# Kernel tuning notes

Hardware: AMD Instinct MI355X
Metric: run time of the kernel (lower is better)

Reference implementation:

```python
import jax, jax.numpy as jnp
import numpy as np

B, L, D = 32, 2048, 512
MODES = 32
H = 1           # num_head
E = D // H      # per-head channels
KMA = 128       # moving_avg kernel
EPS = 1e-5


def setup_inputs() -> dict:
    key = jax.random.key(0)
    ks = jax.random.split(key, 12)
    scale = 1.0 / (D * D)
    lin = lambda k, fi, fo: jax.random.uniform(k, (fo, fi), jnp.float32, -1, 1) / np.sqrt(fi)
    return {
        "x": jax.random.normal(ks[0], (B, L, D), jnp.float32),
        "W_in": lin(ks[1], D, H * E),
        "b_in": jnp.zeros((H * E,), jnp.float32),
        "Wf_r": scale * jax.random.uniform(ks[2], (H, E, E, MODES), jnp.float32),
        "Wf_i": scale * jax.random.uniform(ks[3], (H, E, E, MODES), jnp.float32),
        "W_out": lin(ks[4], H * E, D),
        "b_out": jnp.zeros((D,), jnp.float32),
        "W_conv1": lin(ks[5], D, D),
        "W_conv2": lin(ks[6], D, D),
        "bn_gamma": jnp.ones((L,), jnp.float32),
        "bn_beta": jnp.zeros((L,), jnp.float32),
    }


def moving_average(x, k):
    # x: (b, l, c); replicate-pad front/end exactly as the torch module, then avg-pool k/stride 1
    front = jnp.repeat(x[:, :1, :], k - 1 - (k - 1) // 2, axis=1)
    end = jnp.repeat(x[:, -1:, :], (k - 1) // 2, axis=1)
    xp = jnp.concatenate([front, x, end], axis=1)          # (b, l+k-1, c)
    cs = jnp.cumsum(xp, axis=1)
    cs = jnp.concatenate([jnp.zeros_like(cs[:, :1]), cs], axis=1)
    return (cs[:, k:] - cs[:, :-k]) / k                    # (b, l, c)


def reference(x, W_in, b_in, Wf_r, Wf_i, W_out, b_out, W_conv1, W_conv2, bn_gamma, bn_beta):
    b, l, d = x.shape
    # in projection -> (b, l, h, e) -> (b, h, e, l)
    q = x @ W_in.T + b_in
    q = q.reshape(b, l, H, E).transpose(0, 2, 3, 1)
    # FourierBlock: rfft over time, keep lowest MODES modes, complex mix, irfft
    x_ft = jnp.fft.rfft(q, axis=-1)                        # (b, h, e, l//2+1)
    Wf = (Wf_r + 1j * Wf_i).astype(x_ft.dtype)             # (h, e, e, m)
    out_modes = jnp.einsum('bhim,hiom->bhom', x_ft[..., :MODES], Wf)
    out_ft = jnp.pad(out_modes, ((0, 0), (0, 0), (0, 0), (0, l // 2 + 1 - MODES)))
    fre = jnp.fft.irfft(out_ft, n=l, axis=-1)              # (b, h, e, l)
    # (b, h, e, l) -> (b, l, h*e), out projection (dropout is eval-mode identity)
    fre = fre.transpose(0, 3, 1, 2).reshape(b, l, H * E)
    fre = fre @ W_out.T + b_out
    xr = x + fre
    # series decomposition 1: keep residual
    xr = xr - moving_average(xr, KMA)
    # conv1x1 -> gelu -> conv1x1 (exact erf gelu, matching F.gelu default)
    y = jax.nn.gelu(jnp.einsum('bld,ed->ble', xr, W_conv1), approximate=False)
    y = jnp.einsum('bld,ed->ble', y, W_conv2)
    res = xr + y
    # BatchNorm1d(in_len): channel axis is the time axis, batch stats over (b, d)
    mean = res.mean(axis=(0, 2), keepdims=True)
    var = ((res - mean) ** 2).mean(axis=(0, 2), keepdims=True)
    out = bn_gamma[None, :, None] * (res - mean) / jnp.sqrt(var + EPS) + bn_beta[None, :, None]
    return out
```

## Files before the change

kernel.cpp:

```cpp
#include <hip/hip_runtime.h>
#include <hip/hip_bf16.h>
#include <math.h>

#define B_   32
#define L_   2048
#define D_   512
#define BLROWS (B_*L_)
#define NBIG ((size_t)BLROWS * D_)

typedef __hip_bfloat16 bf16;
using bf16x8 = __attribute__((ext_vector_type(8))) short;
using f32x4  = __attribute__((ext_vector_type(4))) float;

__device__ __forceinline__ unsigned short f2b(float f) {
  bf16 h = __float2bfloat16(f);
  return *reinterpret_cast<unsigned short*>(&h);
}
__device__ __forceinline__ float b2f(unsigned short u) {
  union { unsigned int i; float f; } c;
  c.i = ((unsigned int)u) << 16;
  return c.f;
}

__device__ __forceinline__ void gl_lds16(const void* g, void* l) {
  __builtin_amdgcn_global_load_lds(
      (const __attribute__((address_space(1))) void*)g,
      (__attribute__((address_space(3))) void*)l, 16, 0, 0);
}

__global__ __launch_bounds__(256) void f2bfK(const float4* __restrict__ src,
                                             ushort4* __restrict__ dst,
                                             size_t n4) {
  for (size_t i = (size_t)blockIdx.x * 256 + threadIdx.x; i < n4;
       i += (size_t)gridDim.x * 256) {
    float4 v = src[i];
    ushort4 o;
    o.x = f2b(v.x); o.y = f2b(v.y); o.z = f2b(v.z); o.w = f2b(v.w);
    dst[i] = o;
  }
}

__global__ __launch_bounds__(256) void genTwCS(bf16* __restrict__ TwCS) {
  int idx = blockIdx.x * 256 + threadIdx.x;
  int mrow = idx >> 11, l = idx & 2047;
  int m = mrow & 31;
  int r = (m * l) & (L_ - 1);
  float ang = (float)r * (6.283185307179586f / (float)L_);
  TwCS[idx] = __float2bfloat16((mrow < 32) ? cosf(ang) : -sinf(ang));
}

__global__ __launch_bounds__(256) void genTbF(float* __restrict__ Tb) {
  int idx = blockIdx.x * 256 + threadIdx.x;
  int l = idx >> 6, j = idx & 63;
  int m = j >> 1;
  int r = (m * l) & (L_ - 1);
  float ang = (float)r * (6.283185307179586f / (float)L_);
  Tb[idx] = (j & 1) ? sinf(ang) : cosf(ang);
}

__global__ __launch_bounds__(256) void genTbDbf(const float* __restrict__ Tb,
                                                bf16* __restrict__ TbD) {
  int idx = blockIdx.x * 256 + threadIdx.x;
  int l = idx >> 6, j = idx & 63;
  float s = 0.f;
  for (int t = l - 64; t < l + 64; t++) {
    int cl = min(max(t, 0), L_ - 1);
    s += Tb[cl * 64 + j];
  }
  TbD[idx] = __float2bfloat16(Tb[idx] - s * (1.f / 128.f));
}

__global__ __launch_bounds__(256) void twWf2(const float* __restrict__ Wfr,
                                             const float* __restrict__ Wfi,
                                             bf16* __restrict__ Wcat2) {
  __shared__ __align__(16) bf16 st[256 * 72];
  const int t = threadIdx.x;
  const int i0 = blockIdx.x * 64, o0 = blockIdx.y * 8;
  const int arr = blockIdx.z;
  const float* src = arr ? Wfi : Wfr;
#pragma unroll
  for (int s8 = 0; s8 < 8; s8++) {
    unsigned short v[8];
#pragma unroll
    for (int ss = 0; ss < 8; ss++)
      v[ss] = f2b(src[(size_t)(i0 + s8 * 8 + ss) * 16384 + o0 * 32 + t]);
    int4 wv;
    wv.x = (int)v[0] | ((int)v[1] << 16);
    wv.y = (int)v[2] | ((int)v[3] << 16);
    wv.z = (int)v[4] | ((int)v[5] << 16);
    wv.w = (int)v[6] | ((int)v[7] << 16);
    *(int4*)&st[t * 72 + s8 * 8] = wv;
  }
  __syncthreads();
#pragma unroll
  for (int p = 0; p < 8; p++) {
    const int om = p * 32 + (t >> 3), c = t & 7;
    const int o = om >> 5, m = om & 31;
    int4 rv = *(const int4*)&st[om * 72 + c * 8];
    bf16* dst = Wcat2 + (size_t)m * 524288 + (size_t)(o0 + o) * 1024 +
                arr * 512 + i0 + c * 8;
    *(int4*)dst = rv;
  }
}

template <bool GELU, bool RESID, bool BIAS, bool OUTBF, bool RESBF, bool AFP32,
          bool DFTE>
__global__ __launch_bounds__(256) void gemm_k64(
    const void* __restrict__ Av, const bf16* __restrict__ Wt,
    const float* __restrict__ bias, const void* __restrict__ resid,
    void* __restrict__ Cout, int M, int N, int K,
    const bf16* __restrict__ TwCS, bf16* __restrict__ Pdft) {
  __shared__ __align__(16) bf16 As[2][128 * 64];
  __shared__ __align__(16) bf16 Bs[2][128 * 64];
  const int t = threadIdx.x;
  const int lane = t & 63;
  const int w = t >> 6, wr = w >> 1, wc = w & 1;

  const int id = blockIdx.x;
  const int xcd = id & 7, rest = id >> 3;
  const int cb = rest & 3, rg = rest >> 2;
  const int row0 = (rg * 8 + xcd) * 128, col0 = cb * 128;

  const bf16* Ab = (const bf16*)Av;
  const float* Af = (const float*)Av;

  f32x4 acc[4][4];
#pragma unroll
  for (int i = 0; i < 4; i++)
#pragma unroll
    for (int j = 0; j < 4; j++) acc[i][j] = (f32x4){0.f, 0.f, 0.f, 0.f};

  auto stage = [&](int buf, int k0) {
#pragma unroll
    for (int s = 0; s < 4; s++) {
      const int ci = s * 256 + t;
      const int row = ci >> 3;
      const int cg = ci & 7;
      const int pc = cg ^ (row & 7);
      if (AFP32) {
        const float* ax = Af + (size_t)(row0 + row) * K + k0 + cg * 8;
        float4 v0 = *(const float4*)(ax);
        float4 v1 = *(const float4*)(ax + 4);
        int4 wv;
        wv.x = (int)f2b(v0.x) | ((int)f2b(v0.y) << 16);
        wv.y = (int)f2b(v0.z) | ((int)f2b(v0.w) << 16);
        wv.z = (int)f2b(v1.x) | ((int)f2b(v1.y) << 16);
        wv.w = (int)f2b(v1.z) | ((int)f2b(v1.w) << 16);
        *(int4*)&As[buf][(size_t)(row * 8 + pc) * 8] = wv;
      } else {
        const int kqg = cg ^ (row & 7);
        bf16* dA = &As[buf][(size_t)(s * 256 + (t & ~63)) * 8];
        gl_lds16(Ab + (size_t)(row0 + row) * K + k0 + kqg * 8, dA);
      }
      {
        const int kqg = cg ^ (row & 7);
        bf16* dB = &Bs[buf][(size_t)(s * 256 + (t & ~63)) * 8];
        gl_lds16(Wt + (size_t)(col0 + row) * K + k0 + kqg * 8, dB);
      }
    }
  };

  stage(0, 0);
  int cur = 0;
  for (int k0 = 0; k0 < K; k0 += 64) {
    __syncthreads();
    if (k0 + 64 < K) stage(cur ^ 1, k0 + 64);
#pragma unroll
    for (int ks = 0; ks < 2; ks++) {
      const int c = ks * 4 + (lane >> 4);
      const int pc = c ^ (lane & 7);
      bf16x8 af[4], bg[4];
#pragma unroll
      for (int m = 0; m < 4; m++) {
        const int ra = wr * 64 + m * 16 + (lane & 15);
        af[m] = *reinterpret_cast<const bf16x8*>(&As[cur][(ra * 8 + pc) * 8]);
      }
#pragma unroll
      for (int n = 0; n < 4; n++) {
        const int rb = wc * 64 + n * 16 + (lane & 15);
        bg[n] = *reinterpret_cast<const bf16x8*>(&Bs[cur][(rb * 8 + pc) * 8]);
      }
#pragma unroll
      for (int n = 0; n < 4; n++)
#pragma unroll
        for (int m = 0; m < 4; m++)
          acc[n][m] = __builtin_amdgcn_mfma_f32_16x16x32_bf16(
              bg[n], af[m], acc[n][m], 0, 0, 0);
    }
    cur ^= 1;
  }

  if (DFTE) {
    bf16* QT = (bf16*)As;
    __syncthreads();
#pragma unroll
    for (int n = 0; n < 4; n++) {
      const int ibase = wc * 64 + n * 16 + ((lane >> 4) << 2);
      float4 bsv = *(const float4*)(bias + col0 + ibase);
#pragma unroll
      for (int m = 0; m < 4; m++) {
        const int lloc = wr * 64 + m * 16 + (lane & 15);
#pragma unroll
        for (int j = 0; j < 4; j++) {
          const int iloc = ibase + j;
          float u = acc[n][m][j] + (&bsv.x)[j];
          QT[iloc * 128 + (((lloc >> 3) ^ (iloc & 7)) << 3) + (lloc & 7)] =
              __float2bfloat16(u);
        }
      }
    }
    __syncthreads();
    const int bidx = row0 >> 11, lblk = (row0 >> 7) & 15;
    const int l0g = row0 & 2047;
    f32x4 accd[4][2];
#pragma unroll
    for (int mp = 0; mp < 4; mp++)
#pragma unroll
      for (int ip = 0; ip < 2; ip++) accd[mp][ip] = (f32x4){0.f,0.f,0.f,0.f};
#pragma unroll
    for (int kc = 0; kc < 4; kc++) {
      bf16x8 bgt[4], afq[2];
#pragma unroll
      for (int mp = 0; mp < 4; mp++)
        bgt[mp] = *reinterpret_cast<const bf16x8*>(
            TwCS + (size_t)(mp * 16 + (lane & 15)) * 2048 + l0g + kc * 32 +
            (lane >> 4) * 8);
#pragma unroll
      for (int ip = 0; ip < 2; ip++) {
        const int iloc = (w * 2 + ip) * 16 + (lane & 15);
        const int kchunk = kc * 4 + (lane >> 4);
        const int pcq = kchunk ^ (iloc & 7);
        afq[ip] = *reinterpret_cast<const bf16x8*>(&QT[iloc * 128 + pcq * 8]);
      }
#pragma unroll
      for (int mp = 0; mp < 4; mp++)
#pragma unroll
        for (int ip = 0; ip < 2; ip++)
          accd[mp][ip] = __builtin_amdgcn_mfma_f32_16x16x32_bf16(
              bgt[mp], afq[ip], accd[mp][ip], 0, 0, 0);
    }
    bf16* Pb = Pdft + (size_t)(bidx * 16 + lblk) * 64 * 512;
#pragma unroll
    for (int mp = 0; mp < 4; mp++)
#pragma unroll
      for (int ip = 0; ip < 2; ip++)
#pragma unroll
        for (int j = 0; j < 4; j++) {
          const int mrow = mp * 16 + ((lane >> 4) << 2) + j;
          const int ig = col0 + (w * 2 + ip) * 16 + (lane & 15);
          Pb[(size_t)mrow * 512 + ig] = __float2bfloat16(accd[mp][ip][j]);
        }
    return;
  }

  float* Cf = (float*)Cout;
  ushort* Cb = (ushort*)Cout;
#pragma unroll
  for (int n = 0; n < 4; n++) {
    const int dbase = col0 + wc * 64 + n * 16 + ((lane >> 4) << 2);
    float4 bsv = {0.f, 0.f, 0.f, 0.f};
    if (BIAS) bsv = *(const float4*)(bias + dbase);
#pragma unroll
    for (int m = 0; m < 4; m++) {
      const size_t r = (size_t)row0 + wr * 64 + m * 16 + (lane & 15);
      float v[4];
#pragma unroll
      for (int j = 0; j < 4; j++) {
        float u = acc[n][m][j] + (BIAS ? (&bsv.x)[j] : 0.f);
        if (GELU) u = 0.5f * u * (1.0f + erff(u * 0.70710678118654752f));
        v[j] = u;
      }
      if (RESID) {
        if (RESBF) {
          ushort4 rv = *(const ushort4*)((const ushort*)resid + r * N + dbase);
          v[0] += b2f(rv.x); v[1] += b2f(rv.y);
          v[2] += b2f(rv.z); v[3] += b2f(rv.w);
        } else {
          float4 rv = *(const float4*)((const float*)resid + r * N + dbase);
          v[0] += rv.x; v[1] += rv.y; v[2] += rv.z; v[3] += rv.w;
        }
      }
      if (OUTBF) {
        ushort4 o = {f2b(v[0]), f2b(v[1]), f2b(v[2]), f2b(v[3])};
        *(ushort4*)(Cb + r * N + dbase) = o;
      } else {
        float4 o = {v[0], v[1], v[2], v[3]};
        *(float4*)(Cf + r * N + dbase) = o;
      }
    }
  }
}

__global__ __launch_bounds__(256) void gemmD(
    const bf16* __restrict__ TbD, const bf16* __restrict__ CCT,
    const ushort* __restrict__ u, ushort* __restrict__ xr) {
  __shared__ __align__(16) bf16 As[128 * 64];
  __shared__ __align__(16) bf16 Bs[128 * 64];
  const int t = threadIdx.x;
  const int lane = t & 63;
  const int wid = t >> 6, wr = wid >> 1, wc = wid & 1;
  const int row0 = blockIdx.x * 128, col0 = blockIdx.y * 128;
  const int b = blockIdx.z;
  const bf16* Bsrc = CCT + (size_t)b * 512 * 64;

  const int srow = t >> 3, schk = t & 7;
  const int wb16 = (t & ~63) * 8;
#pragma unroll
  for (int p = 0; p < 4; p++) {
    gl_lds16(TbD + (size_t)(row0 + srow + 32 * p) * 64 + schk * 8,
             &As[p * 2048 + wb16]);
    gl_lds16(Bsrc + (size_t)(col0 + srow + 32 * p) * 64 + schk * 8,
             &Bs[p * 2048 + wb16]);
  }
  __syncthreads();

  f32x4 acc[4][4];
#pragma unroll
  for (int i = 0; i < 4; i++)
#pragma unroll
    for (int j = 0; j < 4; j++) acc[i][j] = (f32x4){0.f, 0.f, 0.f, 0.f};

#pragma unroll
  for (int ks = 0; ks < 2; ks++) {
    bf16x8 af[4], bg[4];
#pragma unroll
    for (int m = 0; m < 4; m++)
      af[m] = *reinterpret_cast<const bf16x8*>(
          &As[(wr * 64 + m * 16 + (lane & 15)) * 64 + ks * 32 +
              (lane >> 4) * 8]);
#pragma unroll
    for (int n = 0; n < 4; n++)
      bg[n] = *reinterpret_cast<const bf16x8*>(
          &Bs[(wc * 64 + n * 16 + (lane & 15)) * 64 + ks * 32 +
              (lane >> 4) * 8]);
#pragma unroll
    for (int n = 0; n < 4; n++)
#pragma unroll
      for (int m = 0; m < 4; m++)
        acc[n][m] = __builtin_amdgcn_mfma_f32_16x16x32_bf16(bg[n], af[m],
                                                            acc[n][m], 0, 0, 0);
  }

#pragma unroll
  for (int n = 0; n < 4; n++) {
    const int dbase = col0 + wc * 64 + n * 16 + ((lane >> 4) << 2);
#pragma unroll
    for (int m = 0; m < 4; m++) {
      const int l = row0 + wr * 64 + m * 16 + (lane & 15);
      const size_t rg = ((size_t)b * L_ + l) * D_ + dbase;
      ushort4 uv = *(const ushort4*)(u + rg);
      ushort4 o;
      o.x = f2b(acc[n][m][0] + b2f(uv.x));
      o.y = f2b(acc[n][m][1] + b2f(uv.y));
      o.z = f2b(acc[n][m][2] + b2f(uv.z));
      o.w = f2b(acc[n][m][3] + b2f(uv.w));
      *(ushort4*)(xr + rg) = o;
    }
  }
}

template <bool BIAS, bool OUTBF, bool MGUARD, int EPI>
__global__ __launch_bounds__(256) void gemm_bt(
    const bf16* __restrict__ A, const bf16* __restrict__ Wt,
    const float* __restrict__ bias, void* __restrict__ Cout,
    int M, int N, int K, long batchA, long batchB, long batchC,
    int ldc, int coff) {
  __shared__ __align__(16) bf16 As[2][128 * 32];
  __shared__ __align__(16) bf16 Bs[2][128 * 32];
  const int t = threadIdx.x;
  const int lane = t & 63;
  const int wid = t >> 6, wr = wid >> 1, wc = wid & 1;
  const int row0 = blockIdx.x * 128, col0 = blockIdx.y * 128;
  const int zb = blockIdx.z;
  A += (size_t)zb * (size_t)batchA;
  Wt += (size_t)zb * (size_t)batchB;

  f32x4 acc[4][4];
#pragma unroll
  for (int i = 0; i < 4; i++)
#pragma unroll
    for (int j = 0; j < 4; j++) acc[i][j] = (f32x4){0.f, 0.f, 0.f, 0.f};

  const int srow = t >> 2, scq = t & 3;
  const int sa0 = MGUARD ? (srow & 31) : srow;
  const int sa1 = MGUARD ? (srow & 31) : (64 + srow);
  const int wbase = (t & ~63) * 8;

  auto stage = [&](int buf, int k0) {
    gl_lds16(A + (size_t)(row0 + sa0) * K + k0 + scq * 8, &As[buf][wbase]);
    gl_lds16(A + (size_t)(row0 + sa1) * K + k0 + scq * 8,
             &As[buf][2048 + wbase]);
    gl_lds16(Wt + (size_t)(col0 + srow) * K + k0 + scq * 8, &Bs[buf][wbase]);
    gl_lds16(Wt + (size_t)(col0 + 64 + srow) * K + k0 + scq * 8,
             &Bs[buf][2048 + wbase]);
  };

  stage(0, 0);
  int cur = 0;
  for (int k0 = 0; k0 < K; k0 += 32) {
    __syncthreads();
    if (k0 + 32 < K) stage(cur ^ 1, k0 + 32);
    bf16x8 af[4], bg[4];
#pragma unroll
    for (int m = 0; m < 4; m++)
      af[m] = *reinterpret_cast<const bf16x8*>(
          &As[cur][(wr * 64 + m * 16 + (lane & 15)) * 32 + (lane >> 4) * 8]);
#pragma unroll
    for (int n = 0; n < 4; n++)
      bg[n] = *reinterpret_cast<const bf16x8*>(
          &Bs[cur][(wc * 64 + n * 16 + (lane & 15)) * 32 + (lane >> 4) * 8]);
#pragma unroll
    for (int m = 0; m < 4; m++)
#pragma unroll
      for (int n = 0; n < 4; n++)
        acc[m][n] = __builtin_amdgcn_mfma_f32_16x16x32_bf16(af[m], bg[n],
                                                            acc[m][n], 0, 0, 0);
    cur ^= 1;
  }

  if (EPI == 3 || EPI == 4) {
    bf16* Cb = (bf16*)Cout;
#pragma unroll
    for (int n = 0; n < 4; n++) {
      int col = col0 + wc * 64 + n * 16 + (lane & 15);
#pragma unroll
      for (int m = 0; m < 4; m++) {
#pragma unroll
        for (int j = 0; j < 4; j++) {
          int row = row0 + wr * 64 + m * 16 + (lane >> 4) * 4 + j;
          int bb = row >> 5, mm = row & 31;
          float scale = (EPI == 3)
              ? ((mm == 0) ? (1.f / (float)L_) : (2.f / (float)L_))
              : (-2.f / (float)L_);
          Cb[((size_t)bb * 512 + col) * 64 + 2 * mm + (EPI == 4 ? 1 : 0)] =
              __float2bfloat16(acc[m][n][j] * scale);
        }
      }
    }
    return;
  }

  float* Cf = (float*)Cout;
  bf16* Cb = (bf16*)Cout;
  const size_t cbase = (size_t)zb * (size_t)batchC;
#pragma unroll
  for (int n = 0; n < 4; n++) {
    int col = col0 + wc * 64 + n * 16 + (lane & 15);
    float bs = 0.f;
    if (BIAS) bs = bias[col];
#pragma unroll
    for (int m = 0; m < 4; m++) {
#pragma unroll
      for (int j = 0; j < 4; j++) {
        int row = row0 + wr * 64 + m * 16 + (lane >> 4) * 4 + j;
        if (MGUARD && row >= M) continue;
        float v = acc[m][n][j] + bs;
        size_t idx = cbase + (size_t)row * ldc + coff + col;
        if (OUTBF) Cb[idx] = __float2bfloat16(v);
        else Cf[idx] = v;
      }
    }
  }
}

__global__ __launch_bounds__(256) void reduceXFT(
    const bf16* __restrict__ Pdft,
    bf16* __restrict__ Aneg, bf16* __restrict__ Aswap) {
  const int b = blockIdx.x, ic = blockIdx.y;
  const int i0 = ic * 64;
#pragma unroll
  for (int s = 0; s < 8; s++) {
    int flat = s * 256 + threadIdx.x;
    int m = flat >> 6, i = flat & 63;
    float sr = 0.f, si = 0.f;
#pragma unroll
    for (int lb = 0; lb < 16; lb++) {
      const bf16* base = Pdft + (size_t)(b * 16 + lb) * 64 * 512;
      sr += b2f(*(const unsigned short*)&base[(size_t)m * 512 + i0 + i]);
      si += b2f(*(const unsigned short*)&base[(size_t)(32 + m) * 512 + i0 + i]);
    }
    size_t ab = ((size_t)m * B_ + b) * 1024;
    Aneg[ab + i0 + i] = __float2bfloat16(sr);
    Aneg[ab + 512 + i0 + i] = __float2bfloat16(-si);
    Aswap[ab + i0 + i] = __float2bfloat16(si);
    Aswap[ab + 512 + i0 + i] = __float2bfloat16(sr);
  }
}

__global__ __launch_bounds__(256) void stageE(const float* __restrict__ in,
                                              bf16* __restrict__ outbf) {
  const int b = blockIdx.x, dg = blockIdx.y, lc = blockIdx.z;
  const int d = dg * 256 + threadIdx.x;
  const float* col = in + (size_t)b * L_ * D_ + d;
  bf16* bcol = outbf + (size_t)b * L_ * D_ + d;
  const int l0 = lc * 128;
  float Wsum = 0.f;
  for (int s = l0 - 64; s < l0 + 64; s++) {
    int cl = min(max(s, 0), L_ - 1);
    Wsum += col[(size_t)cl * D_];
  }
  for (int l = l0; l < l0 + 128; l++) {
    float v = col[(size_t)l * D_];
    bcol[(size_t)l * D_] = __float2bfloat16(v - Wsum * (1.f / 128.f));
    int fa = min(l + 64, L_ - 1);
    int fb = max(l - 64, 0);
    Wsum += col[(size_t)fa * D_] - col[(size_t)fb * D_];
  }
}

__global__ __launch_bounds__(256) void bnStats(const ushort* __restrict__ res,
                                               float* __restrict__ meanb,
                                               float* __restrict__ rstdb) {
  const int l = blockIdx.x;
  const int t = threadIdx.x;
  float s = 0.f, s2 = 0.f;
  for (int b = 0; b < B_; b++) {
    const ushort* p = res + ((size_t)b * L_ + l) * D_ + 2 * t;
    ushort2 v2 = *(const ushort2*)p;
    float a = b2f(v2.x), c = b2f(v2.y);
    s += a + c;
    s2 += a * a + c * c;
  }
#pragma unroll
  for (int off = 32; off > 0; off >>= 1) {
    s += __shfl_down(s, off, 64);
    s2 += __shfl_down(s2, off, 64);
  }
  __shared__ float shs[4], shs2[4];
  int wid = t >> 6;
  if ((t & 63) == 0) { shs[wid] = s; shs2[wid] = s2; }
  __syncthreads();
  if (t == 0) {
    float S = shs[0] + shs[1] + shs[2] + shs[3];
    float S2 = shs2[0] + shs2[1] + shs2[2] + shs2[3];
    const float inv = 1.f / (float)(B_ * D_);
    float mean = S * inv;
    float var = S2 * inv - mean * mean;
    meanb[l] = mean;
    rstdb[l] = rsqrtf(var + 1e-5f);
  }
}

__global__ __launch_bounds__(256) void bnApply(
    const ushort* __restrict__ res, const float* __restrict__ gamma,
    const float* __restrict__ beta, const float* __restrict__ meanb,
    const float* __restrict__ rstdb, float* __restrict__ out) {
  size_t idx = (size_t)blockIdx.x * 256 + threadIdx.x;
  if (idx >= NBIG / 4) return;
  size_t e = idx * 4;
  int l = (int)((e >> 9) & (L_ - 1));
  ushort4 v = *(const ushort4*)(res + e);
  float m = meanb[l], rs = rstdb[l];
  float g = gamma[l] * rs, bt = beta[l];
  float4 o;
  o.x = (b2f(v.x) - m) * g + bt;
  o.y = (b2f(v.y) - m) * g + bt;
  o.z = (b2f(v.z) - m) * g + bt;
  o.w = (b2f(v.w) - m) * g + bt;
  *(float4*)(out + e) = o;
}

extern "C" void kernel_launch(void* const* d_in, const int* in_sizes, int n_in,
                              void* d_out, int out_size, void* d_ws,
                              size_t ws_size, hipStream_t stream) {
  const float* x      = (const float*)d_in[0];
  const float* W_in   = (const float*)d_in[1];
  const float* b_in   = (const float*)d_in[2];
  const float* Wf_r   = (const float*)d_in[3];
  const float* Wf_i   = (const float*)d_in[4];
  const float* W_out  = (const float*)d_in[5];
  const float* b_out  = (const float*)d_in[6];
  const float* W_c1   = (const float*)d_in[7];
  const float* W_c2   = (const float*)d_in[8];
  const float* gamma  = (const float*)d_in[9];
  const float* beta   = (const float*)d_in[10];
  float* outp = (float*)d_out;
  (void)b_out;

  float* f = (float*)d_ws;
  float* buf0 = f;
  bf16*  resbf = (bf16*)buf0;
  bf16*  Pdft  = (bf16*)buf0;
  bf16*  Wcat2 = Pdft + (size_t)512 * 64 * 512;
  bf16*  Woutbf= Wcat2 + (size_t)32 * 512 * 1024;
  bf16*  Aneg  = Woutbf + 262144;
  bf16*  Aswap = Aneg + 1048576;
  bf16*  OMr   = Aswap + 1048576;
  bf16*  OMi   = OMr + 524288;
  bf16*  CCT   = OMi + 524288;
  bf16*  TwCS  = (bf16*)(f + NBIG);
  float* TbF   = (float*)(TwCS + 131072);
  bf16*  TbD   = (bf16*)(TbF + 131072);
  bf16*  Wibf  = TbD + 131072;
  bf16*  W1bf  = Wibf + 262144;
  bf16*  W2bf  = W1bf + 262144;
  float* meanb = (float*)(W2bf + 262144);
  float* rstdb = meanb + L_;

  bf16* ubf  = ((bf16*)d_out) + NBIG;
  bf16* xrbf = (bf16*)d_out;
  bf16* y1bf = ubf;

  genTwCS<<<512, 256, 0, stream>>>(TwCS);
  genTbF<<<512, 256, 0, stream>>>(TbF);
  genTbDbf<<<512, 256, 0, stream>>>(TbF, TbD);
  f2bfK<<<256, 256, 0, stream>>>((const float4*)W_in, (ushort4*)Wibf, 65536);
  f2bfK<<<256, 256, 0, stream>>>((const float4*)W_c1, (ushort4*)W1bf, 65536);
  f2bfK<<<256, 256, 0, stream>>>((const float4*)W_c2, (ushort4*)W2bf, 65536);
  f2bfK<<<256, 256, 0, stream>>>((const float4*)W_out, (ushort4*)Woutbf, 65536);
  twWf2<<<dim3(8, 64, 2), 256, 0, stream>>>(Wf_r, Wf_i, Wcat2);

  gemm_k64<false, false, true, false, false, true, true>
      <<<2048, 256, 0, stream>>>(
      x, Wibf, b_in, nullptr, nullptr, BLROWS, D_, D_, TwCS, Pdft);

  reduceXFT<<<dim3(B_, 8), 256, 0, stream>>>(Pdft, Aneg, Aswap);

  gemm_bt<false, true, true, 0><<<dim3(1, 4, 32), 256, 0, stream>>>(
      Aneg, Wcat2, nullptr, OMr, 32, 512, 1024, 32768, 524288, 512, 16384, 0);
  gemm_bt<false, true, true, 0><<<dim3(1, 4, 32), 256, 0, stream>>>(
      Aswap, Wcat2, nullptr, OMi, 32, 512, 1024, 32768, 524288, 512, 16384, 0);

  gemm_bt<false, true, false, 3><<<dim3(8, 4, 1), 256, 0, stream>>>(
      OMr, Woutbf, nullptr, CCT, 1024, 512, 512, 0, 0, 0, 0, 0);
  gemm_bt<false, true, false, 4><<<dim3(8, 4, 1), 256, 0, stream>>>(
      OMi, Woutbf, nullptr, CCT, 1024, 512, 512, 0, 0, 0, 0, 0);

  stageE<<<dim3(B_, 2, 16), 256, 0, stream>>>(x, ubf);

  gemmD<<<dim3(16, 4, 32), 256, 0, stream>>>(TbD, CCT, (const ushort*)ubf,
                                             (ushort*)xrbf);

  gemm_k64<true, false, false, true, false, false, false>
      <<<2048, 256, 0, stream>>>(
      xrbf, W1bf, nullptr, nullptr, y1bf, BLROWS, D_, D_, nullptr, nullptr);

  gemm_k64<false, true, false, true, true, false, false>
      <<<2048, 256, 0, stream>>>(
      y1bf, W2bf, nullptr, xrbf, resbf, BLROWS, D_, D_, nullptr, nullptr);

  bnStats<<<L_, 256, 0, stream>>>((const ushort*)resbf, meanb, rstdb);
  bnApply<<<(NBIG / 4 + 255) / 256, 256, 0, stream>>>(
      (const ushort*)resbf, gamma, beta, meanb, rstdb, outp);
}
```

Measured before the change: 600.0 us.

## Use 8 waves per block in 128x128 GEMM tiles with smaller per-wave subtiles

The three big GEMM kernels now launch 512 threads per block instead of 256. Each wave computes a 32x64 subtile instead of 64x64, and the fused DFT epilogue now handles one 16-column slice per wave instead of two. Staging loops are split across more threads. The aim is more waves in flight to hide latency and lower register pressure per wave. The cost is fewer MFMAs per LDS fragment load, so operand reuse per wave drops.

```diff
diff --git a/kernel.cpp b/kernel.cpp
--- a/kernel.cpp
+++ b/kernel.cpp
@@ -105,7 +105,7 @@
 
 template <bool GELU, bool RESID, bool BIAS, bool OUTBF, bool RESBF, bool AFP32,
           bool DFTE>
-__global__ __launch_bounds__(256) void gemm_k64(
+__global__ __launch_bounds__(512) void gemm_k64(
     const void* __restrict__ Av, const bf16* __restrict__ Wt,
     const float* __restrict__ bias, const void* __restrict__ resid,
     void* __restrict__ Cout, int M, int N, int K,
@@ -114,7 +114,8 @@
   __shared__ __align__(16) bf16 Bs[2][128 * 64];
   const int t = threadIdx.x;
   const int lane = t & 63;
-  const int w = t >> 6, wr = w >> 1, wc = w & 1;
+  const int w = t >> 6;
+  const int wr = w >> 1, wc = w & 1;
 
   const int id = blockIdx.x;
   const int xcd = id & 7, rest = id >> 3;
@@ -124,16 +125,16 @@
   const bf16* Ab = (const bf16*)Av;
   const float* Af = (const float*)Av;
 
-  f32x4 acc[4][4];
+  f32x4 acc[4][2];
 #pragma unroll
   for (int i = 0; i < 4; i++)
 #pragma unroll
-    for (int j = 0; j < 4; j++) acc[i][j] = (f32x4){0.f, 0.f, 0.f, 0.f};
+    for (int j = 0; j < 2; j++) acc[i][j] = (f32x4){0.f, 0.f, 0.f, 0.f};
 
   auto stage = [&](int buf, int k0) {
 #pragma unroll
-    for (int s = 0; s < 4; s++) {
-      const int ci = s * 256 + t;
+    for (int s = 0; s < 2; s++) {
+      const int ci = s * 512 + t;
       const int row = ci >> 3;
       const int cg = ci & 7;
       const int pc = cg ^ (row & 7);
@@ -149,12 +150,12 @@
         *(int4*)&As[buf][(size_t)(row * 8 + pc) * 8] = wv;
       } else {
         const int kqg = cg ^ (row & 7);
-        bf16* dA = &As[buf][(size_t)(s * 256 + (t & ~63)) * 8];
+        bf16* dA = &As[buf][(size_t)(s * 512 + (t & ~63)) * 8];
         gl_lds16(Ab + (size_t)(row0 + row) * K + k0 + kqg * 8, dA);
       }
       {
         const int kqg = cg ^ (row & 7);
-        bf16* dB = &Bs[buf][(size_t)(s * 256 + (t & ~63)) * 8];
+        bf16* dB = &Bs[buf][(size_t)(s * 512 + (t & ~63)) * 8];
         gl_lds16(Wt + (size_t)(col0 + row) * K + k0 + kqg * 8, dB);
       }
     }
@@ -169,10 +170,10 @@
     for (int ks = 0; ks < 2; ks++) {
       const int c = ks * 4 + (lane >> 4);
       const int pc = c ^ (lane & 7);
-      bf16x8 af[4], bg[4];
-#pragma unroll
-      for (int m = 0; m < 4; m++) {
-        const int ra = wr * 64 + m * 16 + (lane & 15);
+      bf16x8 af[2], bg[4];
+#pragma unroll
+      for (int m = 0; m < 2; m++) {
+        const int ra = wr * 32 + m * 16 + (lane & 15);
         af[m] = *reinterpret_cast<const bf16x8*>(&As[cur][(ra * 8 + pc) * 8]);
       }
 #pragma unroll
@@ -183,7 +184,7 @@
 #pragma unroll
       for (int n = 0; n < 4; n++)
 #pragma unroll
-        for (int m = 0; m < 4; m++)
+        for (int m = 0; m < 2; m++)
           acc[n][m] = __builtin_amdgcn_mfma_f32_16x16x32_bf16(
               bg[n], af[m], acc[n][m], 0, 0, 0);
     }
@@ -198,8 +199,8 @@
       const int ibase = wc * 64 + n * 16 + ((lane >> 4) << 2);
       float4 bsv = *(const float4*)(bias + col0 + ibase);
 #pragma unroll
-      for (int m = 0; m < 4; m++) {
-        const int lloc = wr * 64 + m * 16 + (lane & 15);
+      for (int m = 0; m < 2; m++) {
+        const int lloc = wr * 32 + m * 16 + (lane & 15);
 #pragma unroll
         for (int j = 0; j < 4; j++) {
           const int iloc = ibase + j;
@@ -212,44 +213,37 @@
     __syncthreads();
     const int bidx = row0 >> 11, lblk = (row0 >> 7) & 15;
     const int l0g = row0 & 2047;
-    f32x4 accd[4][2];
-#pragma unroll
-    for (int mp = 0; mp < 4; mp++)
-#pragma unroll
-      for (int ip = 0; ip < 2; ip++) accd[mp][ip] = (f32x4){0.f,0.f,0.f,0.f};
+    f32x4 accd[4];
+#pragma unroll
+    for (int mp = 0; mp < 4; mp++) accd[mp] = (f32x4){0.f, 0.f, 0.f, 0.f};
+    const int iloc = w * 16 + (lane & 15);
 #pragma unroll
     for (int kc = 0; kc < 4; kc++) {
-      bf16x8 bgt[4], afq[2];
+      bf16x8 bgt[4], afq;
 #pragma unroll
       for (int mp = 0; mp < 4; mp++)
         bgt[mp] = *reinterpret_cast<const bf16x8*>(
             TwCS + (size_t)(mp * 16 + (lane & 15)) * 2048 + l0g + kc * 32 +
             (lane >> 4) * 8);
-#pragma unroll
-      for (int ip = 0; ip < 2; ip++) {
-        const int iloc = (w * 2 + ip) * 16 + (lane & 15);
+      {
         const int kchunk = kc * 4 + (lane >> 4);
         const int pcq = kchunk ^ (iloc & 7);
-        afq[ip] = *reinterpret_cast<const bf16x8*>(&QT[iloc * 128 + pcq * 8]);
+        afq = *reinterpret_cast<const bf16x8*>(&QT[iloc * 128 + pcq * 8]);
       }
 #pragma unroll
       for (int mp = 0; mp < 4; mp++)
-#pragma unroll
-        for (int ip = 0; ip < 2; ip++)
-          accd[mp][ip] = __builtin_amdgcn_mfma_f32_16x16x32_bf16(
-              bgt[mp], afq[ip], accd[mp][ip], 0, 0, 0);
+        accd[mp] = __builtin_amdgcn_mfma_f32_16x16x32_bf16(
+            bgt[mp], afq, accd[mp], 0, 0, 0);
     }
     bf16* Pb = Pdft + (size_t)(bidx * 16 + lblk) * 64 * 512;
 #pragma unroll
     for (int mp = 0; mp < 4; mp++)
 #pragma unroll
-      for (int ip = 0; ip < 2; ip++)
-#pragma unroll
-        for (int j = 0; j < 4; j++) {
-          const int mrow = mp * 16 + ((lane >> 4) << 2) + j;
-          const int ig = col0 + (w * 2 + ip) * 16 + (lane & 15);
-          Pb[(size_t)mrow * 512 + ig] = __float2bfloat16(accd[mp][ip][j]);
-        }
+      for (int j = 0; j < 4; j++) {
+        const int mrow = mp * 16 + ((lane >> 4) << 2) + j;
+        const int ig = col0 + iloc;
+        Pb[(size_t)mrow * 512 + ig] = __float2bfloat16(accd[mp][j]);
+      }
     return;
   }
 
@@ -261,8 +255,8 @@
     float4 bsv = {0.f, 0.f, 0.f, 0.f};
     if (BIAS) bsv = *(const float4*)(bias + dbase);
 #pragma unroll
-    for (int m = 0; m < 4; m++) {
-      const size_t r = (size_t)row0 + wr * 64 + m * 16 + (lane & 15);
+    for (int m = 0; m < 2; m++) {
+      const size_t r = (size_t)row0 + wr * 32 + m * 16 + (lane & 15);
       float v[4];
 #pragma unroll
       for (int j = 0; j < 4; j++) {
@@ -611,7 +605,7 @@
   twWf2<<<dim3(8, 64, 2), 256, 0, stream>>>(Wf_r, Wf_i, Wcat2);
 
   gemm_k64<false, false, true, false, false, true, true>
-      <<<2048, 256, 0, stream>>>(
+      <<<2048, 512, 0, stream>>>(
       x, Wibf, b_in, nullptr, nullptr, BLROWS, D_, D_, TwCS, Pdft);
 
   reduceXFT<<<dim3(B_, 8), 256, 0, stream>>>(Pdft, Aneg, Aswap);
@@ -632,11 +626,11 @@
                                              (ushort*)xrbf);
 
   gemm_k64<true, false, false, true, false, false, false>
-      <<<2048, 256, 0, stream>>>(
+      <<<2048, 512, 0, stream>>>(
       xrbf, W1bf, nullptr, nullptr, y1bf, BLROWS, D_, D_, nullptr, nullptr);
 
   gemm_k64<false, true, false, true, true, false, false>
-      <<<2048, 256, 0, stream>>>(
+      <<<2048, 512, 0, stream>>>(
       y1bf, W2bf, nullptr, xrbf, resbf, BLROWS, D_, D_, nullptr, nullptr);
 
   bnStats<<<L_, 256, 0, stream>>>((const ushort*)resbf, meanb, rstdb);
```

New measurement: 556.6 us, median of 2. -7.2%, faster.
